# Optimization experiments

Hardware: AMD Instinct MI355X
Metric: run time of the kernel (lower is better)

## Reference

```python
import jax, jax.numpy as jnp
import numpy as np

B, H, D = 64, 256, 768          # news items, hidden_dim, text feature dim
NR, ER = 100000, 400000          # repost nodes/edges
NC, EC, G = 100000, 300000, 512  # comment nodes/edges, comment graphs


def gcn_conv(x, src, dst, W):
    """PyG GCNConv (bias=False): sym-normalized A+I, then linear. Matches
    out = D^-1/2 (A+I) D^-1/2 X W with unit edge weights."""
    n = x.shape[0]
    loop = jnp.arange(n, dtype=src.dtype)
    s = jnp.concatenate([src, loop])
    d = jnp.concatenate([dst, loop])
    deg = jnp.zeros((n,), x.dtype).at[d].add(1.0)  # >=1 due to self loops
    dinv = jax.lax.rsqrt(deg)
    h = x @ W
    msg = h[s] * (dinv[s] * dinv[d])[:, None]
    return jax.ops.segment_sum(msg, d, num_segments=n)


def gcn_encoder(x, edge_index, W1, W2):
    src, dst = edge_index[0], edge_index[1]
    h = jax.nn.relu(gcn_conv(x, src, dst, W1))  # dropout is identity in eval
    return gcn_conv(h, src, dst, W2)


def mean_pool(x, seg, num_segments):
    s = jax.ops.segment_sum(x, seg, num_segments=num_segments)
    cnt = jax.ops.segment_sum(jnp.ones((x.shape[0],), x.dtype), seg,
                              num_segments=num_segments)
    return s / jnp.maximum(cnt, 1.0)[:, None]


def setup_inputs() -> dict:
    key = jax.random.key(0)
    ks = jax.random.split(key, 24)
    f = lambda k, shp: jax.random.normal(k, shp, dtype=jnp.float32)
    w = lambda k, shp: jax.random.normal(k, shp, dtype=jnp.float32) * 0.02
    inp = {
        "content": f(ks[0], (B, D)),
        "video": f(ks[1], (B, D)),
        "image": f(ks[2], (B, D)),
        "repost_x": f(ks[3], (NR, D)),
        "comment_x": f(ks[4], (NC, D)),
        "W_text": w(ks[5], (D, H)),
        "W_video": w(ks[6], (D, H)),
        "W_image": w(ks[7], (D, H)),
        "Wr1": w(ks[8], (H, H)),
        "Wr2": w(ks[9], (H, H)),
        "Wc1": w(ks[10], (H, H)),
        "Wc2": w(ks[11], (H, H)),
        "W1": w(ks[12], (5 * H, H)),
        "b1": jnp.zeros((H,), jnp.float32),
        "W2": w(ks[13], (H, 2)),
        "b2": jnp.zeros((2,), jnp.float32),
        "repost_edge_index": jax.random.randint(ks[14], (2, ER), 0, NR, dtype=jnp.int32),
        "repost_batch": jnp.sort(jax.random.randint(ks[15], (NR,), 0, B, dtype=jnp.int32)),
        "comment_edge_index": jax.random.randint(ks[16], (2, EC), 0, NC, dtype=jnp.int32),
        "comment_batch": jnp.sort(jax.random.randint(ks[17], (NC,), 0, G, dtype=jnp.int32)),
        "comment_graph_batch": jnp.sort(jax.random.randint(ks[18], (G,), 0, B, dtype=jnp.int32)),
        "label": jax.random.randint(ks[19], (B,), 0, 2, dtype=jnp.int32),
    }
    return inp


def reference(content, video, image, repost_x, comment_x,
              W_text, W_video, W_image, Wr1, Wr2, Wc1, Wc2,
              W1, b1, W2, b2,
              repost_edge_index, repost_batch,
              comment_edge_index, comment_batch, comment_graph_batch,
              label):
    content_reps = content @ W_text                         # [B,H]
    # repost branch
    rx = repost_x @ W_text                                  # [NR,H]
    rr = gcn_encoder(rx, repost_edge_index, Wr1, Wr2)
    repost_reps = mean_pool(rr, repost_batch, B)            # [B,H]
    # comment branch: nodes -> comment graphs -> news items
    cx = comment_x @ W_text                                 # [NC,H]
    cr = gcn_encoder(cx, comment_edge_index, Wc1, Wc2)
    graphs_reps = mean_pool(cr, comment_batch, G)           # [G,H]
    comment_reps = mean_pool(graphs_reps, comment_graph_batch, B)  # [B,H]
    # modality branches (dropout identity in eval)
    video_reps = video @ W_video
    image_reps = image @ W_image
    reps = jnp.concatenate([content_reps, repost_reps, comment_reps,
                            video_reps, image_reps], axis=-1)  # [B,5H]
    h = jax.nn.relu(reps @ W1 + b1)
    preds = h @ W2 + b2                                      # [B,2]
    logp = jax.nn.log_softmax(preds, axis=-1)
    loss = -jnp.mean(jnp.take_along_axis(logp, label[:, None].astype(jnp.int32), axis=-1))
    return preds, loss
```

## Files before the change

kernel.cpp:

```cpp
#include <hip/hip_runtime.h>
#include <hip/hip_bf16.h>

typedef __bf16 bfr;
typedef bfr v8bf __attribute__((ext_vector_type(8)));
typedef bfr v4bf __attribute__((ext_vector_type(4)));
typedef float v4f __attribute__((ext_vector_type(4)));

static constexpr int Bn = 64, H = 256, D = 768;
static constexpr int NR = 100000, ER = 400000;
static constexpr int NC = 100000, EC = 300000, G = 512;
static constexpr int SCAN_CH = 1024;

__global__ void fill_f32(float* p, float v, int n) {
  int i = blockIdx.x * blockDim.x + threadIdx.x;
  if (i < n) p[i] = v;
}
__global__ void fill_i32(int* p, int v, int n) {
  int i = blockIdx.x * blockDim.x + threadIdx.x;
  if (i < n) p[i] = v;
}

__global__ void transpose_w(const float* __restrict__ W, bfr* __restrict__ Wt,
                            int K, int N) {
  int i = blockIdx.x * blockDim.x + threadIdx.x;
  if (i >= K * N) return;
  int k = i / N, n = i - k * N;
  Wt[(size_t)n * K + k] = (bfr)W[i];
}

template<typename TA>
__launch_bounds__(256)
__global__ void gemm_k(const TA* __restrict__ A, const bfr* __restrict__ Bt,
                       bfr* __restrict__ Cb, float* __restrict__ Cf,
                       int M, int K, int ldc, int col0) {
  int wid = (int)((blockIdx.x * 256u + threadIdx.x) >> 6);
  int m0 = wid * 16;
  if (m0 >= M) return;
  int lane = threadIdx.x & 63;
  int mrow = lane & 15;
  int quad = lane >> 4;
  const TA* Ap = A + (size_t)(m0 + mrow) * K + quad * 8;
  const bfr* Bp = Bt + (size_t)mrow * K + quad * 8;
  v4f acc[16] = {};
  for (int k0 = 0; k0 < K; k0 += 32) {
    v8bf a;
    if constexpr (sizeof(TA) == 4) {
      const float4* p = (const float4*)(Ap + k0);
      float4 x = p[0], y = p[1];
      a[0] = (bfr)x.x; a[1] = (bfr)x.y; a[2] = (bfr)x.z; a[3] = (bfr)x.w;
      a[4] = (bfr)y.x; a[5] = (bfr)y.y; a[6] = (bfr)y.z; a[7] = (bfr)y.w;
    } else {
      a = *(const v8bf*)(Ap + k0);
    }
#pragma unroll
    for (int nt = 0; nt < 16; ++nt) {
      v8bf b = *(const v8bf*)(Bp + (size_t)nt * 16 * K + k0);
      acc[nt] = __builtin_amdgcn_mfma_f32_16x16x32_bf16(a, b, acc[nt], 0, 0, 0);
    }
  }
#pragma unroll
  for (int nt = 0; nt < 16; ++nt) {
#pragma unroll
    for (int r = 0; r < 4; ++r) {
      int row = m0 + quad * 4 + r;
      int col = col0 + nt * 16 + mrow;
      float v = acc[nt][r];
      if (Cf) Cf[(size_t)row * ldc + col] = v;
      else    Cb[(size_t)row * ldc + col] = (bfr)v;
    }
  }
}

static constexpr int TBM = 128, TBN = 256, TBK = 32;

__device__ __forceinline__ void gld_lds16(const void* g, void* l) {
  __builtin_amdgcn_global_load_lds(
      (const __attribute__((address_space(1))) void*)g,
      (__attribute__((address_space(3))) void*)l, 16, 0, 0);
}

template<typename TA>
__launch_bounds__(512)
__global__ void gemm_tile(const TA* __restrict__ A, const bfr* __restrict__ Bt,
                          bfr* __restrict__ C, int M, int K) {
  __shared__ bfr As[TBM * TBK];
  __shared__ bfr Bs[TBN * TBK];
  int m0 = blockIdx.x * TBM;
  int t = threadIdx.x;
  int lane = t & 63;
  int w = t >> 6;
  int wm = w >> 2;
  int wn = w & 3;
  int mrow = lane & 15;
  int quad = lane >> 4;

  int rA = t >> 2, ccA = t & 3;
  int rgA = m0 + rA; if (rgA >= M) rgA = M - 1;
  const TA* gA = A + (size_t)rgA * K + ccA * 8;
  int rB0 = t >> 2, ccB = t & 3;
  const bfr* gB0 = Bt + (size_t)rB0 * K + ccB * 8;
  const bfr* gB1 = Bt + (size_t)(128 + rB0) * K + ccB * 8;
  bfr* lA  = As + (size_t)(w * 64) * 8;
  bfr* lB0 = Bs + (size_t)(w * 64) * 8;
  bfr* lB1 = Bs + (size_t)(512 + w * 64) * 8;

  const bfr* pA = As + (size_t)(wm * 64 + mrow) * TBK + quad * 8;
  const bfr* pB = Bs + (size_t)(wn * 64 + mrow) * TBK + quad * 8;

  v4f acc[4][4] = {};
  for (int k0 = 0; k0 < K; k0 += TBK) {
    if constexpr (sizeof(TA) == 2) {
      gld_lds16(gA, lA);
    } else {
      const float4* p = (const float4*)gA;
      float4 x = p[0], y = p[1];
      v8bf v;
      v[0] = (bfr)x.x; v[1] = (bfr)x.y; v[2] = (bfr)x.z; v[3] = (bfr)x.w;
      v[4] = (bfr)y.x; v[5] = (bfr)y.y; v[6] = (bfr)y.z; v[7] = (bfr)y.w;
      *(v8bf*)(As + (size_t)t * 8) = v;
    }
    gld_lds16(gB0, lB0);
    gld_lds16(gB1, lB1);
    gA += TBK; gB0 += TBK; gB1 += TBK;
    __syncthreads();

    v8bf af[4], bfv[4];
#pragma unroll
    for (int i = 0; i < 4; ++i)
      af[i] = *(const v8bf*)(pA + (size_t)i * 16 * TBK);
#pragma unroll
    for (int i = 0; i < 4; ++i)
      bfv[i] = *(const v8bf*)(pB + (size_t)i * 16 * TBK);
#pragma unroll
    for (int mi = 0; mi < 4; ++mi)
#pragma unroll
      for (int ni = 0; ni < 4; ++ni)
        acc[mi][ni] = __builtin_amdgcn_mfma_f32_16x16x32_bf16(
            af[mi], bfv[ni], acc[mi][ni], 0, 0, 0);
    __syncthreads();
  }

#pragma unroll
  for (int mi = 0; mi < 4; ++mi) {
#pragma unroll
    for (int ni = 0; ni < 4; ++ni) {
#pragma unroll
      for (int r = 0; r < 4; ++r) {
        int row = m0 + wm * 64 + mi * 16 + quad * 4 + r;
        int col = wn * 64 + ni * 16 + mrow;
        if (row < M) C[(size_t)row * H + col] = (bfr)acc[mi][ni][r];
      }
    }
  }
}

__global__ void deg_count_i(const int* __restrict__ dst, int* deg, int E) {
  int e = blockIdx.x * blockDim.x + threadIdx.x;
  if (e < E) atomicAdd(deg + dst[e], 1);
}
__global__ void dinv_from_deg(const int* __restrict__ deg, float* dinv, int n) {
  int i = blockIdx.x * blockDim.x + threadIdx.x;
  if (i < n) dinv[i] = rsqrtf((float)deg[i] + 1.0f);
}

__global__ void scan1(const int* __restrict__ deg, int* __restrict__ part,
                      int* __restrict__ bsum, int n) {
  __shared__ int tmp[256];
  int t = threadIdx.x;
  int base = blockIdx.x * SCAN_CH + t * 4;
  int v0 = (base + 0 < n) ? deg[base + 0] : 0;
  int v1 = (base + 1 < n) ? deg[base + 1] : 0;
  int v2 = (base + 2 < n) ? deg[base + 2] : 0;
  int v3 = (base + 3 < n) ? deg[base + 3] : 0;
  int ls = v0 + v1 + v2 + v3;
  tmp[t] = ls;
  __syncthreads();
  for (int o = 1; o < 256; o <<= 1) {
    int vv = (t >= o) ? tmp[t - o] : 0;
    __syncthreads();
    tmp[t] += vv;
    __syncthreads();
  }
  int off = tmp[t] - ls;
  if (base + 0 < n) part[base + 0] = off;
  if (base + 1 < n) part[base + 1] = off + v0;
  if (base + 2 < n) part[base + 2] = off + v0 + v1;
  if (base + 3 < n) part[base + 3] = off + v0 + v1 + v2;
  if (t == 255) bsum[blockIdx.x] = tmp[255];
}
__global__ void scan2(int* bsum, int nb) {
  if (threadIdx.x == 0 && blockIdx.x == 0) {
    int run = 0;
    for (int b = 0; b < nb; ++b) { int s = bsum[b]; bsum[b] = run; run += s; }
  }
}
__global__ void scan3(int* __restrict__ part, const int* __restrict__ bsum,
                      int n, int E) {
  int i = blockIdx.x * blockDim.x + threadIdx.x;
  if (i < n) part[i] += bsum[i / SCAN_CH];
  if (i == n) part[n] = E;
}

__global__ void fill_edges(const int* __restrict__ src, const int* __restrict__ dst,
                           const float* __restrict__ dinv, const int* __restrict__ rp,
                           int* __restrict__ cursor, int* __restrict__ esrc,
                           float* __restrict__ ew, int E) {
  int e = blockIdx.x * blockDim.x + threadIdx.x;
  if (e >= E) return;
  int s = src[e], d = dst[e];
  int pos = rp[d] + atomicAdd(cursor + d, 1);
  esrc[pos] = s;
  ew[pos] = dinv[s] * dinv[d];
}

__device__ __forceinline__ void bf4_to_f32(const ushort4 u, float f[4]) {
  f[0] = __uint_as_float((unsigned)u.x << 16);
  f[1] = __uint_as_float((unsigned)u.y << 16);
  f[2] = __uint_as_float((unsigned)u.z << 16);
  f[3] = __uint_as_float((unsigned)u.w << 16);
}
template<bool RELU>
__launch_bounds__(256)
__global__ void gcn_gather(const bfr* __restrict__ h, const int* __restrict__ rp,
                           const int* __restrict__ esrc, const float* __restrict__ ew,
                           const float* __restrict__ dinv,
                           bfr* __restrict__ outB, float* __restrict__ outF, int N) {
  int node = (int)((blockIdx.x * 256u + threadIdx.x) >> 6);
  if (node >= N) return;
  int lane = threadIdx.x & 63;
  const ushort* hp = (const ushort*)h;
  size_t self = (size_t)node * H + lane * 4;
  float di = dinv[node];
  float w0 = di * di;
  float a[4], f[4];
  bf4_to_f32(*(const ushort4*)(hp + self), f);
  a[0] = f[0] * w0; a[1] = f[1] * w0; a[2] = f[2] * w0; a[3] = f[3] * w0;
  int beg = rp[node], end = rp[node + 1];
  for (int j = beg; j < end; ++j) {
    int s = esrc[j];
    float wj = ew[j];
    bf4_to_f32(*(const ushort4*)(hp + (size_t)s * H + lane * 4), f);
    a[0] += f[0] * wj; a[1] += f[1] * wj; a[2] += f[2] * wj; a[3] += f[3] * wj;
  }
  if (RELU) {
    v4bf o;
    o[0] = (bfr)fmaxf(a[0], 0.0f); o[1] = (bfr)fmaxf(a[1], 0.0f);
    o[2] = (bfr)fmaxf(a[2], 0.0f); o[3] = (bfr)fmaxf(a[3], 0.0f);
    *(v4bf*)(outB + self) = o;
  } else {
    float4 o = make_float4(a[0], a[1], a[2], a[3]);
    *(float4*)(outF + self) = o;
  }
}

__global__ void pool_seg(const float* __restrict__ x, const int* __restrict__ seg,
                         int n, float* __restrict__ out, int ldo, int col0) {
  int s = blockIdx.x;
  int t = threadIdx.x;
  int lo = 0, hi = n;
  while (lo < hi) { int m = (lo + hi) >> 1; if (seg[m] < s) lo = m + 1; else hi = m; }
  int beg = lo;
  hi = n;
  while (lo < hi) { int m = (lo + hi) >> 1; if (seg[m] < s + 1) lo = m + 1; else hi = m; }
  int end = lo;
  float a0 = 0, a1 = 0, a2 = 0, a3 = 0;
  int r = beg;
  for (; r + 4 <= end; r += 4) {
    a0 += x[(size_t)(r + 0) * H + t];
    a1 += x[(size_t)(r + 1) * H + t];
    a2 += x[(size_t)(r + 2) * H + t];
    a3 += x[(size_t)(r + 3) * H + t];
  }
  for (; r < end; ++r) a0 += x[(size_t)r * H + t];
  float acc = (a0 + a1) + (a2 + a3);
  out[(size_t)s * ldo + col0 + t] = acc / fmaxf((float)(end - beg), 1.0f);
}

__launch_bounds__(256)
__global__ void final_mlp(const float* __restrict__ reps, const float* __restrict__ W1,
                          const float* __restrict__ b1, const float* __restrict__ W2,
                          const float* __restrict__ b2, const int* __restrict__ label,
                          float* __restrict__ out, float* __restrict__ loss_acc) {
  __shared__ float r[5 * H];
  __shared__ float h[H];
  __shared__ float pr[2];
  int b = blockIdx.x;
  int t = threadIdx.x;
  for (int i = t; i < 5 * H; i += 256) r[i] = reps[(size_t)b * (5 * H) + i];
  __syncthreads();
  float acc = b1[t];
  for (int k = 0; k < 5 * H; ++k) acc += r[k] * W1[(size_t)k * H + t];
  h[t] = fmaxf(acc, 0.0f);
  __syncthreads();
  if (t < 2) {
    float p = b2[t];
    for (int k = 0; k < H; ++k) p += h[k] * W2[k * 2 + t];
    pr[t] = p;
  }
  __syncthreads();
  if (t == 0) {
    float p0 = pr[0], p1 = pr[1];
    out[b * 2 + 0] = p0;
    out[b * 2 + 1] = p1;
    float m = fmaxf(p0, p1);
    float lse = m + logf(expf(p0 - m) + expf(p1 - m));
    float lp = (label[b] ? p1 : p0) - lse;
    atomicAdd(loss_acc, -lp * (1.0f / 64.0f));
  }
}
__global__ void loss_write(const float* loss_acc, float* out) {
  out[128] = *loss_acc;
}

extern "C" void kernel_launch(void* const* d_in, const int* in_sizes, int n_in,
                              void* d_out, int out_size, void* d_ws, size_t ws_size,
                              hipStream_t stream) {
  const float* content   = (const float*)d_in[0];
  const float* video     = (const float*)d_in[1];
  const float* image     = (const float*)d_in[2];
  const float* repost_x  = (const float*)d_in[3];
  const float* comment_x = (const float*)d_in[4];
  const float* W_text    = (const float*)d_in[5];
  const float* W_video   = (const float*)d_in[6];
  const float* W_image   = (const float*)d_in[7];
  const float* Wr1       = (const float*)d_in[8];
  const float* Wr2       = (const float*)d_in[9];
  const float* Wc1       = (const float*)d_in[10];
  const float* Wc2       = (const float*)d_in[11];
  const float* W1        = (const float*)d_in[12];
  const float* b1        = (const float*)d_in[13];
  const float* W2        = (const float*)d_in[14];
  const float* b2        = (const float*)d_in[15];
  const int* r_edge      = (const int*)d_in[16];
  const int* r_batch     = (const int*)d_in[17];
  const int* c_edge      = (const int*)d_in[18];
  const int* c_batch     = (const int*)d_in[19];
  const int* cg_batch    = (const int*)d_in[20];
  const int* label       = (const int*)d_in[21];
  float* out = (float*)d_out;

  char* wsb = (char*)d_ws;
  size_t off = 0;
  auto alloc = [&](size_t bytes) -> void* {
    void* p = wsb + off;
    off += (bytes + 255) & ~(size_t)255;
    return p;
  };
  const size_t NH = (size_t)NR * H;
  bfr*   bufA    = (bfr*)alloc(NH * 2);
  bfr*   bufB    = (bfr*)alloc(NH * 2);
  float* bufC    = (float*)alloc(NH * 4);
  float* dinv    = (float*)alloc(NR * 4);
  int*   deg     = (int*)alloc(NR * 4);
  int*   cursor  = (int*)alloc(NR * 4);
  int*   row_ptr = (int*)alloc((NR + 1) * 4);
  int*   esrc    = (int*)alloc((size_t)ER * 4);
  float* ew      = (float*)alloc((size_t)ER * 4);
  int*   bsum    = (int*)alloc(128 * 4);
  bfr*   Wt_t    = (bfr*)alloc((size_t)D * H * 2);
  bfr*   Wt_v    = (bfr*)alloc((size_t)D * H * 2);
  bfr*   Wt_i    = (bfr*)alloc((size_t)D * H * 2);
  bfr*   Wt_r1   = (bfr*)alloc((size_t)H * H * 2);
  bfr*   Wt_r2   = (bfr*)alloc((size_t)H * H * 2);
  bfr*   Wt_c1   = (bfr*)alloc((size_t)H * H * 2);
  bfr*   Wt_c2   = (bfr*)alloc((size_t)H * H * 2);
  float* reps    = (float*)alloc((size_t)Bn * 5 * H * 4);
  float* graphs  = (float*)alloc((size_t)G * H * 4);
  float* lossw   = (float*)alloc(4);
  (void)ws_size; (void)n_in; (void)in_sizes; (void)out_size;

  const int T = 256;
  auto cdiv = [](int a, int b) { return (a + b - 1) / b; };

  transpose_w<<<cdiv(D * H, T), T, 0, stream>>>(W_text, Wt_t, D, H);
  transpose_w<<<cdiv(D * H, T), T, 0, stream>>>(W_video, Wt_v, D, H);
  transpose_w<<<cdiv(D * H, T), T, 0, stream>>>(W_image, Wt_i, D, H);
  transpose_w<<<cdiv(H * H, T), T, 0, stream>>>(Wr1, Wt_r1, H, H);
  transpose_w<<<cdiv(H * H, T), T, 0, stream>>>(Wr2, Wt_r2, H, H);
  transpose_w<<<cdiv(H * H, T), T, 0, stream>>>(Wc1, Wt_c1, H, H);
  transpose_w<<<cdiv(H * H, T), T, 0, stream>>>(Wc2, Wt_c2, H, H);
  fill_f32<<<1, 1, 0, stream>>>(lossw, 0.0f, 1);

  auto gemm_small = [&](const float* A, const bfr* Bt, float* Cf,
                        int M, int K, int ldc, int col0) {
    gemm_k<float><<<cdiv(M / 16, 4), T, 0, stream>>>(A, Bt, nullptr, Cf, M, K, ldc, col0);
  };
  auto gemm_big_f = [&](const float* A, const bfr* Bt, bfr* C, int M, int K) {
    gemm_tile<float><<<cdiv(M, TBM), 512, 0, stream>>>(A, Bt, C, M, K);
  };
  auto gemm_big_b = [&](const bfr* A, const bfr* Bt, bfr* C, int M, int K) {
    gemm_tile<bfr><<<cdiv(M, TBM), 512, 0, stream>>>(A, Bt, C, M, K);
  };
  auto build_csr = [&](const int* edge, int N, int E) {
    int nb = cdiv(N, SCAN_CH);
    fill_i32<<<cdiv(N, T), T, 0, stream>>>(deg, 0, N);
    deg_count_i<<<cdiv(E, T), T, 0, stream>>>(edge + E, deg, E);
    dinv_from_deg<<<cdiv(N, T), T, 0, stream>>>(deg, dinv, N);
    scan1<<<nb, T, 0, stream>>>(deg, row_ptr, bsum, N);
    scan2<<<1, 64, 0, stream>>>(bsum, nb);
    scan3<<<cdiv(N + 1, T), T, 0, stream>>>(row_ptr, bsum, N, E);
    fill_i32<<<cdiv(N, T), T, 0, stream>>>(cursor, 0, N);
    fill_edges<<<cdiv(E, T), T, 0, stream>>>(edge, edge + E, dinv, row_ptr,
                                             cursor, esrc, ew, E);
  };
  auto gather_relu = [&](const bfr* h, bfr* o, int N) {
    gcn_gather<true><<<cdiv(N, 4), T, 0, stream>>>(h, row_ptr, esrc, ew, dinv,
                                                   o, nullptr, N);
  };
  auto gather_f32 = [&](const bfr* h, float* o, int N) {
    gcn_gather<false><<<cdiv(N, 4), T, 0, stream>>>(h, row_ptr, esrc, ew, dinv,
                                                    nullptr, o, N);
  };

  gemm_small(content, Wt_t, reps, Bn, D, 5 * H, 0 * H);
  gemm_small(video,   Wt_v, reps, Bn, D, 5 * H, 3 * H);
  gemm_small(image,   Wt_i, reps, Bn, D, 5 * H, 4 * H);

  gemm_big_f(repost_x, Wt_t, bufA, NR, D);
  build_csr(r_edge, NR, ER);
  gemm_big_b(bufA, Wt_r1, bufB, NR, H);
  gather_relu(bufB, bufA, NR);
  gemm_big_b(bufA, Wt_r2, bufB, NR, H);
  gather_f32(bufB, bufC, NR);
  pool_seg<<<Bn, H, 0, stream>>>(bufC, r_batch, NR, reps, 5 * H, 1 * H);

  gemm_big_f(comment_x, Wt_t, bufA, NC, D);
  build_csr(c_edge, NC, EC);
  gemm_big_b(bufA, Wt_c1, bufB, NC, H);
  gather_relu(bufB, bufA, NC);
  gemm_big_b(bufA, Wt_c2, bufB, NC, H);
  gather_f32(bufB, bufC, NC);
  pool_seg<<<G, H, 0, stream>>>(bufC, c_batch, NC, graphs, H, 0);
  pool_seg<<<Bn, H, 0, stream>>>(graphs, cg_batch, G, reps, 5 * H, 2 * H);

  final_mlp<<<Bn, T, 0, stream>>>(reps, W1, b1, W2, b2, label, out, lossw);
  loss_write<<<1, 1, 0, stream>>>(lossw, out);
}
```

Baseline: 1.700 ms.

## Double-buffer fp32 GEMM, add resident-B H×H GEMM, fuse prep and CSR kernels

The fp32-input tile GEMM now double-buffers its LDS tiles, prefetching the next K slice of A into registers and B via global_load_lds while the current slice runs through MFMA. H×H bf16 GEMMs move to a new kernel that keeps the whole 256×256 weight in 128KB of LDS and each row's A fragments in registers. Weight transposes, loss zeroing and degree zeroing are merged into one prep kernel. dinv computation and cursor zeroing are folded into the scan kernels, which cuts launch count. The large LDS footprint limits the new GEMM to one block per CU, which reduces occupancy.

```diff
diff --git a/kernel.cpp b/kernel.cpp
--- a/kernel.cpp
+++ b/kernel.cpp
@@ -11,47 +11,59 @@
 static constexpr int NC = 100000, EC = 300000, G = 512;
 static constexpr int SCAN_CH = 1024;
 
-__global__ void fill_f32(float* p, float v, int n) {
-  int i = blockIdx.x * blockDim.x + threadIdx.x;
-  if (i < n) p[i] = v;
-}
-__global__ void fill_i32(int* p, int v, int n) {
-  int i = blockIdx.x * blockDim.x + threadIdx.x;
-  if (i < n) p[i] = v;
-}
-
-__global__ void transpose_w(const float* __restrict__ W, bfr* __restrict__ Wt,
-                            int K, int N) {
-  int i = blockIdx.x * blockDim.x + threadIdx.x;
-  if (i >= K * N) return;
-  int k = i / N, n = i - k * N;
-  Wt[(size_t)n * K + k] = (bfr)W[i];
-}
-
-template<typename TA>
+__global__ void prep_all(const float* __restrict__ Wt0, const float* __restrict__ Wv,
+                         const float* __restrict__ Wi, const float* __restrict__ Wr1,
+                         const float* __restrict__ Wr2, const float* __restrict__ Wc1,
+                         const float* __restrict__ Wc2,
+                         bfr* __restrict__ Ot, bfr* __restrict__ Ov, bfr* __restrict__ Oi,
+                         bfr* __restrict__ Or1, bfr* __restrict__ Or2,
+                         bfr* __restrict__ Oc1, bfr* __restrict__ Oc2,
+                         int* __restrict__ deg_r, int* __restrict__ deg_c,
+                         float* __restrict__ lossw) {
+  int i = blockIdx.x * 256 + threadIdx.x;
+  if (i == 0) *lossw = 0.0f;
+  const int DH = D * H, HH = H * H;
+  if (i < 3 * DH) {
+    int s = i / DH, j = i - s * DH;
+    const float* W = (s == 0) ? Wt0 : (s == 1 ? Wv : Wi);
+    bfr* O = (s == 0) ? Ot : (s == 1 ? Ov : Oi);
+    int k = j / H, n = j - k * H;
+    O[(size_t)n * D + k] = (bfr)W[j];
+    return;
+  }
+  i -= 3 * DH;
+  if (i < 4 * HH) {
+    int s = i / HH, j = i - s * HH;
+    const float* W = (s == 0) ? Wr1 : (s == 1 ? Wr2 : (s == 2 ? Wc1 : Wc2));
+    bfr* O = (s == 0) ? Or1 : (s == 1 ? Or2 : (s == 2 ? Oc1 : Oc2));
+    int k = j / H, n = j - k * H;
+    O[(size_t)n * H + k] = (bfr)W[j];
+    return;
+  }
+  i -= 4 * HH;
+  if (i < NR) { deg_r[i] = 0; return; }
+  i -= NR;
+  if (i < NC) deg_c[i] = 0;
+}
+
 __launch_bounds__(256)
-__global__ void gemm_k(const TA* __restrict__ A, const bfr* __restrict__ Bt,
-                       bfr* __restrict__ Cb, float* __restrict__ Cf,
-                       int M, int K, int ldc, int col0) {
+__global__ void gemm_k(const float* __restrict__ A, const bfr* __restrict__ Bt,
+                       float* __restrict__ Cf, int M, int K, int ldc, int col0) {
   int wid = (int)((blockIdx.x * 256u + threadIdx.x) >> 6);
   int m0 = wid * 16;
   if (m0 >= M) return;
   int lane = threadIdx.x & 63;
   int mrow = lane & 15;
   int quad = lane >> 4;
-  const TA* Ap = A + (size_t)(m0 + mrow) * K + quad * 8;
+  const float* Ap = A + (size_t)(m0 + mrow) * K + quad * 8;
   const bfr* Bp = Bt + (size_t)mrow * K + quad * 8;
   v4f acc[16] = {};
   for (int k0 = 0; k0 < K; k0 += 32) {
     v8bf a;
-    if constexpr (sizeof(TA) == 4) {
-      const float4* p = (const float4*)(Ap + k0);
-      float4 x = p[0], y = p[1];
-      a[0] = (bfr)x.x; a[1] = (bfr)x.y; a[2] = (bfr)x.z; a[3] = (bfr)x.w;
-      a[4] = (bfr)y.x; a[5] = (bfr)y.y; a[6] = (bfr)y.z; a[7] = (bfr)y.w;
-    } else {
-      a = *(const v8bf*)(Ap + k0);
-    }
+    const float4* p = (const float4*)(Ap + k0);
+    float4 x = p[0], y = p[1];
+    a[0] = (bfr)x.x; a[1] = (bfr)x.y; a[2] = (bfr)x.z; a[3] = (bfr)x.w;
+    a[4] = (bfr)y.x; a[5] = (bfr)y.y; a[6] = (bfr)y.z; a[7] = (bfr)y.w;
 #pragma unroll
     for (int nt = 0; nt < 16; ++nt) {
       v8bf b = *(const v8bf*)(Bp + (size_t)nt * 16 * K + k0);
@@ -64,14 +76,10 @@
     for (int r = 0; r < 4; ++r) {
       int row = m0 + quad * 4 + r;
       int col = col0 + nt * 16 + mrow;
-      float v = acc[nt][r];
-      if (Cf) Cf[(size_t)row * ldc + col] = v;
-      else    Cb[(size_t)row * ldc + col] = (bfr)v;
+      Cf[(size_t)row * ldc + col] = acc[nt][r];
     }
   }
 }
-
-static constexpr int TBM = 128, TBN = 256, TBK = 32;
 
 __device__ __forceinline__ void gld_lds16(const void* g, void* l) {
   __builtin_amdgcn_global_load_lds(
@@ -79,92 +87,139 @@
       (__attribute__((address_space(3))) void*)l, 16, 0, 0);
 }
 
-template<typename TA>
+static constexpr int TBM = 128, TBN = 256, TBK = 32;
+
 __launch_bounds__(512)
-__global__ void gemm_tile(const TA* __restrict__ A, const bfr* __restrict__ Bt,
-                          bfr* __restrict__ C, int M, int K) {
-  __shared__ bfr As[TBM * TBK];
-  __shared__ bfr Bs[TBN * TBK];
+__global__ void gemm_tile_f(const float* __restrict__ A, const bfr* __restrict__ Bt,
+                            bfr* __restrict__ C, int M, int K) {
+  __shared__ bfr As[2][TBM * TBK];
+  __shared__ bfr Bs[2][TBN * TBK];
   int m0 = blockIdx.x * TBM;
   int t = threadIdx.x;
   int lane = t & 63;
-  int w = t >> 6;
-  int wm = w >> 2;
-  int wn = w & 3;
-  int mrow = lane & 15;
-  int quad = lane >> 4;
+  int w = t >> 6, wm = w >> 2, wn = w & 3;
+  int mrow = lane & 15, quad = lane >> 4;
 
   int rA = t >> 2, ccA = t & 3;
   int rgA = m0 + rA; if (rgA >= M) rgA = M - 1;
-  const TA* gA = A + (size_t)rgA * K + ccA * 8;
-  int rB0 = t >> 2, ccB = t & 3;
-  const bfr* gB0 = Bt + (size_t)rB0 * K + ccB * 8;
-  const bfr* gB1 = Bt + (size_t)(128 + rB0) * K + ccB * 8;
-  bfr* lA  = As + (size_t)(w * 64) * 8;
-  bfr* lB0 = Bs + (size_t)(w * 64) * 8;
-  bfr* lB1 = Bs + (size_t)(512 + w * 64) * 8;
-
-  const bfr* pA = As + (size_t)(wm * 64 + mrow) * TBK + quad * 8;
-  const bfr* pB = Bs + (size_t)(wn * 64 + mrow) * TBK + quad * 8;
+  const float* gAp = A + (size_t)rgA * K + ccA * 8;
+  int rB = t >> 2, ccB = t & 3;
+  const bfr* gB0 = Bt + (size_t)rB * K + ccB * 8;
+  const bfr* gB1 = Bt + (size_t)(128 + rB) * K + ccB * 8;
+
+  int aoffA = wm * 64 + mrow;
+  int aoffB = wn * 64 + mrow;
+
+  float4 x, y;
+  auto loadA = [&](int k0) {
+    const float4* p = (const float4*)(gAp + k0);
+    x = p[0]; y = p[1];
+  };
+  auto stageB = [&](int buf, int k0) {
+    gld_lds16(gB0 + k0, (char*)&Bs[buf][0] + (size_t)(w * 64) * 16);
+    gld_lds16(gB1 + k0, (char*)&Bs[buf][0] + (size_t)(512 + w * 64) * 16);
+  };
+  auto writeA = [&](int buf) {
+    v8bf v;
+    v[0] = (bfr)x.x; v[1] = (bfr)x.y; v[2] = (bfr)x.z; v[3] = (bfr)x.w;
+    v[4] = (bfr)y.x; v[5] = (bfr)y.y; v[6] = (bfr)y.z; v[7] = (bfr)y.w;
+    *(v8bf*)(&As[buf][0] + (size_t)t * 8) = v;
+  };
+
+  loadA(0); stageB(0, 0); writeA(0);
+  __syncthreads();
 
   v4f acc[4][4] = {};
-  for (int k0 = 0; k0 < K; k0 += TBK) {
-    if constexpr (sizeof(TA) == 2) {
-      gld_lds16(gA, lA);
-    } else {
-      const float4* p = (const float4*)gA;
-      float4 x = p[0], y = p[1];
-      v8bf v;
-      v[0] = (bfr)x.x; v[1] = (bfr)x.y; v[2] = (bfr)x.z; v[3] = (bfr)x.w;
-      v[4] = (bfr)y.x; v[5] = (bfr)y.y; v[6] = (bfr)y.z; v[7] = (bfr)y.w;
-      *(v8bf*)(As + (size_t)t * 8) = v;
-    }
-    gld_lds16(gB0, lB0);
-    gld_lds16(gB1, lB1);
-    gA += TBK; gB0 += TBK; gB1 += TBK;
-    __syncthreads();
-
-    v8bf af[4], bfv[4];
-#pragma unroll
-    for (int i = 0; i < 4; ++i)
-      af[i] = *(const v8bf*)(pA + (size_t)i * 16 * TBK);
-#pragma unroll
-    for (int i = 0; i < 4; ++i)
-      bfv[i] = *(const v8bf*)(pB + (size_t)i * 16 * TBK);
+  int cur = 0;
+  int nsteps = K / TBK;
+  for (int ks = 0; ks < nsteps; ++ks) {
+    int k0n = (ks + 1) * TBK;
+    bool more = k0n < K;
+    if (more) { loadA(k0n); stageB(cur ^ 1, k0n); }
+    const bfr* pA = &As[cur][0] + (size_t)aoffA * TBK + quad * 8;
+    const bfr* pB = &Bs[cur][0] + (size_t)aoffB * TBK + quad * 8;
+    v8bf af[4], bv[4];
+#pragma unroll
+    for (int i2 = 0; i2 < 4; ++i2) af[i2] = *(const v8bf*)(pA + (size_t)i2 * 16 * TBK);
+#pragma unroll
+    for (int i2 = 0; i2 < 4; ++i2) bv[i2] = *(const v8bf*)(pB + (size_t)i2 * 16 * TBK);
 #pragma unroll
     for (int mi = 0; mi < 4; ++mi)
 #pragma unroll
       for (int ni = 0; ni < 4; ++ni)
         acc[mi][ni] = __builtin_amdgcn_mfma_f32_16x16x32_bf16(
-            af[mi], bfv[ni], acc[mi][ni], 0, 0, 0);
+            af[mi], bv[ni], acc[mi][ni], 0, 0, 0);
+    if (more) writeA(cur ^ 1);
     __syncthreads();
-  }
-
-#pragma unroll
-  for (int mi = 0; mi < 4; ++mi) {
-#pragma unroll
-    for (int ni = 0; ni < 4; ++ni) {
+    cur ^= 1;
+  }
+
+#pragma unroll
+  for (int mi = 0; mi < 4; ++mi)
+#pragma unroll
+    for (int ni = 0; ni < 4; ++ni)
 #pragma unroll
       for (int r = 0; r < 4; ++r) {
         int row = m0 + wm * 64 + mi * 16 + quad * 4 + r;
         int col = wn * 64 + ni * 16 + mrow;
         if (row < M) C[(size_t)row * H + col] = (bfr)acc[mi][ni][r];
       }
+}
+
+__launch_bounds__(512, 1)
+__global__ void gemm_pB(const bfr* __restrict__ A, const bfr* __restrict__ Bt,
+                        bfr* __restrict__ C, int M) {
+  __shared__ bfr Bs[65536];
+  int t = threadIdx.x;
+  int lane = t & 63;
+  int w = t >> 6;
+  int mrow = lane & 15, quad = lane >> 4;
+
+#pragma unroll
+  for (int r = 0; r < 16; ++r) {
+    int c = r * 512 + t;
+    int T = c >> 6, cw = c & 63;
+    int kt = T >> 4, nt = T & 15;
+    int tm = cw >> 2, tq = cw & 3;
+    const bfr* src = Bt + (size_t)(nt * 16 + tm) * H + kt * 32 + tq * 8;
+    gld_lds16(src, (char*)Bs + (size_t)(r * 512 + w * 64) * 16);
+  }
+  __syncthreads();
+
+  int row = blockIdx.x * 128 + w * 16 + mrow;
+  int rclamp = row < M ? row : M - 1;
+  const bfr* Ap = A + (size_t)rclamp * H + quad * 8;
+  v8bf a[8];
+#pragma unroll
+  for (int kt = 0; kt < 8; ++kt) a[kt] = *(const v8bf*)(Ap + kt * 32);
+
+  v4f acc[16] = {};
+#pragma unroll
+  for (int kt = 0; kt < 8; ++kt) {
+#pragma unroll
+    for (int nt = 0; nt < 16; ++nt) {
+      v8bf b = *(const v8bf*)(Bs + ((size_t)(kt * 16 + nt) * 64 + mrow * 4 + quad) * 8);
+      acc[nt] = __builtin_amdgcn_mfma_f32_16x16x32_bf16(a[kt], b, acc[nt], 0, 0, 0);
     }
   }
+
+  int orow_base = blockIdx.x * 128 + w * 16 + quad * 4;
+#pragma unroll
+  for (int nt = 0; nt < 16; ++nt)
+#pragma unroll
+    for (int r = 0; r < 4; ++r) {
+      int orow = orow_base + r;
+      if (orow < M) C[(size_t)orow * H + nt * 16 + mrow] = (bfr)acc[nt][r];
+    }
 }
 
 __global__ void deg_count_i(const int* __restrict__ dst, int* deg, int E) {
   int e = blockIdx.x * blockDim.x + threadIdx.x;
   if (e < E) atomicAdd(deg + dst[e], 1);
 }
-__global__ void dinv_from_deg(const int* __restrict__ deg, float* dinv, int n) {
-  int i = blockIdx.x * blockDim.x + threadIdx.x;
-  if (i < n) dinv[i] = rsqrtf((float)deg[i] + 1.0f);
-}
 
 __global__ void scan1(const int* __restrict__ deg, int* __restrict__ part,
-                      int* __restrict__ bsum, int n) {
+                      int* __restrict__ bsum, float* __restrict__ dinv, int n) {
   __shared__ int tmp[256];
   int t = threadIdx.x;
   int base = blockIdx.x * SCAN_CH + t * 4;
@@ -172,6 +227,10 @@
   int v1 = (base + 1 < n) ? deg[base + 1] : 0;
   int v2 = (base + 2 < n) ? deg[base + 2] : 0;
   int v3 = (base + 3 < n) ? deg[base + 3] : 0;
+  if (base + 0 < n) dinv[base + 0] = rsqrtf((float)v0 + 1.0f);
+  if (base + 1 < n) dinv[base + 1] = rsqrtf((float)v1 + 1.0f);
+  if (base + 2 < n) dinv[base + 2] = rsqrtf((float)v2 + 1.0f);
+  if (base + 3 < n) dinv[base + 3] = rsqrtf((float)v3 + 1.0f);
   int ls = v0 + v1 + v2 + v3;
   tmp[t] = ls;
   __syncthreads();
@@ -195,9 +254,9 @@
   }
 }
 __global__ void scan3(int* __restrict__ part, const int* __restrict__ bsum,
-                      int n, int E) {
+                      int* __restrict__ cursor, int n, int E) {
   int i = blockIdx.x * blockDim.x + threadIdx.x;
-  if (i < n) part[i] += bsum[i / SCAN_CH];
+  if (i < n) { part[i] += bsum[i / SCAN_CH]; cursor[i] = 0; }
   if (i == n) part[n] = E;
 }
 
@@ -351,7 +410,8 @@
   bfr*   bufB    = (bfr*)alloc(NH * 2);
   float* bufC    = (float*)alloc(NH * 4);
   float* dinv    = (float*)alloc(NR * 4);
-  int*   deg     = (int*)alloc(NR * 4);
+  int*   deg_r   = (int*)alloc(NR * 4);
+  int*   deg_c   = (int*)alloc(NC * 4);
   int*   cursor  = (int*)alloc(NR * 4);
   int*   row_ptr = (int*)alloc((NR + 1) * 4);
   int*   esrc    = (int*)alloc((size_t)ER * 4);
@@ -372,34 +432,30 @@
   const int T = 256;
   auto cdiv = [](int a, int b) { return (a + b - 1) / b; };
 
-  transpose_w<<<cdiv(D * H, T), T, 0, stream>>>(W_text, Wt_t, D, H);
-  transpose_w<<<cdiv(D * H, T), T, 0, stream>>>(W_video, Wt_v, D, H);
-  transpose_w<<<cdiv(D * H, T), T, 0, stream>>>(W_image, Wt_i, D, H);
-  transpose_w<<<cdiv(H * H, T), T, 0, stream>>>(Wr1, Wt_r1, H, H);
-  transpose_w<<<cdiv(H * H, T), T, 0, stream>>>(Wr2, Wt_r2, H, H);
-  transpose_w<<<cdiv(H * H, T), T, 0, stream>>>(Wc1, Wt_c1, H, H);
-  transpose_w<<<cdiv(H * H, T), T, 0, stream>>>(Wc2, Wt_c2, H, H);
-  fill_f32<<<1, 1, 0, stream>>>(lossw, 0.0f, 1);
+  {
+    int total = 3 * D * H + 4 * H * H + NR + NC;
+    prep_all<<<cdiv(total, T), T, 0, stream>>>(
+        W_text, W_video, W_image, Wr1, Wr2, Wc1, Wc2,
+        Wt_t, Wt_v, Wt_i, Wt_r1, Wt_r2, Wt_c1, Wt_c2,
+        deg_r, deg_c, lossw);
+  }
 
   auto gemm_small = [&](const float* A, const bfr* Bt, float* Cf,
                         int M, int K, int ldc, int col0) {
-    gemm_k<float><<<cdiv(M / 16, 4), T, 0, stream>>>(A, Bt, nullptr, Cf, M, K, ldc, col0);
+    gemm_k<<<cdiv(M / 16, 4), T, 0, stream>>>(A, Bt, Cf, M, K, ldc, col0);
   };
   auto gemm_big_f = [&](const float* A, const bfr* Bt, bfr* C, int M, int K) {
-    gemm_tile<float><<<cdiv(M, TBM), 512, 0, stream>>>(A, Bt, C, M, K);
-  };
-  auto gemm_big_b = [&](const bfr* A, const bfr* Bt, bfr* C, int M, int K) {
-    gemm_tile<bfr><<<cdiv(M, TBM), 512, 0, stream>>>(A, Bt, C, M, K);
-  };
-  auto build_csr = [&](const int* edge, int N, int E) {
+    gemm_tile_f<<<cdiv(M, TBM), 512, 0, stream>>>(A, Bt, C, M, K);
+  };
+  auto gemm_big_b = [&](const bfr* A, const bfr* Bt, bfr* C, int M) {
+    gemm_pB<<<cdiv(M, 128), 512, 0, stream>>>(A, Bt, C, M);
+  };
+  auto build_csr = [&](const int* edge, int* deg, int N, int E) {
     int nb = cdiv(N, SCAN_CH);
-    fill_i32<<<cdiv(N, T), T, 0, stream>>>(deg, 0, N);
     deg_count_i<<<cdiv(E, T), T, 0, stream>>>(edge + E, deg, E);
-    dinv_from_deg<<<cdiv(N, T), T, 0, stream>>>(deg, dinv, N);
-    scan1<<<nb, T, 0, stream>>>(deg, row_ptr, bsum, N);
+    scan1<<<nb, T, 0, stream>>>(deg, row_ptr, bsum, dinv, N);
     scan2<<<1, 64, 0, stream>>>(bsum, nb);
-    scan3<<<cdiv(N + 1, T), T, 0, stream>>>(row_ptr, bsum, N, E);
-    fill_i32<<<cdiv(N, T), T, 0, stream>>>(cursor, 0, N);
+    scan3<<<cdiv(N + 1, T), T, 0, stream>>>(row_ptr, bsum, cursor, N, E);
     fill_edges<<<cdiv(E, T), T, 0, stream>>>(edge, edge + E, dinv, row_ptr,
                                              cursor, esrc, ew, E);
   };
@@ -417,18 +473,18 @@
   gemm_small(image,   Wt_i, reps, Bn, D, 5 * H, 4 * H);
 
   gemm_big_f(repost_x, Wt_t, bufA, NR, D);
-  build_csr(r_edge, NR, ER);
-  gemm_big_b(bufA, Wt_r1, bufB, NR, H);
+  build_csr(r_edge, deg_r, NR, ER);
+  gemm_big_b(bufA, Wt_r1, bufB, NR);
   gather_relu(bufB, bufA, NR);
-  gemm_big_b(bufA, Wt_r2, bufB, NR, H);
+  gemm_big_b(bufA, Wt_r2, bufB, NR);
   gather_f32(bufB, bufC, NR);
   pool_seg<<<Bn, H, 0, stream>>>(bufC, r_batch, NR, reps, 5 * H, 1 * H);
 
   gemm_big_f(comment_x, Wt_t, bufA, NC, D);
-  build_csr(c_edge, NC, EC);
-  gemm_big_b(bufA, Wt_c1, bufB, NC, H);
+  build_csr(c_edge, deg_c, NC, EC);
+  gemm_big_b(bufA, Wt_c1, bufB, NC);
   gather_relu(bufB, bufA, NC);
-  gemm_big_b(bufA, Wt_c2, bufB, NC, H);
+  gemm_big_b(bufA, Wt_c2, bufB, NC);
   gather_f32(bufB, bufC, NC);
   pool_seg<<<G, H, 0, stream>>>(bufC, c_batch, NC, graphs, H, 0);
   pool_seg<<<Bn, H, 0, stream>>>(graphs, cg_batch, G, reps, 5 * H, 2 * H);
```

Measured after the change: 1.701 ms. About the same (+0.1%).
